# Performance work log

Measured on AMD Instinct MI355X. Metric: run time of the kernel, lower is better.

Reference implementation:

```python
import jax, jax.numpy as jnp
import numpy as np

B, S, D, H = 2, 2048, 1024, 16
HD = D // H  # head_dim = 64

def setup_inputs() -> dict:
    key = jax.random.key(0)
    ks = jax.random.split(key, 5)
    scale = 0.02
    return {
        "x":  jax.random.normal(ks[0], (B, S, D), dtype=jnp.float32),
        "Wq": jax.random.normal(ks[1], (D, D), dtype=jnp.float32) * scale,
        "Wk": jax.random.normal(ks[2], (D, D), dtype=jnp.float32) * scale,
        "Wv": jax.random.normal(ks[3], (D, D), dtype=jnp.float32) * scale,
        "Wo": jax.random.normal(ks[4], (D, D), dtype=jnp.float32) * scale,
    }

def reference(x, Wq, Wk, Wv, Wo):
    b, s, d = x.shape
    # projections (bias-free linear): [b,s,d] @ [d,d]
    q = (x @ Wq).reshape(b, s, H, HD).transpose(0, 2, 1, 3)  # [b,h,s,hd]
    k = (x @ Wk).reshape(b, s, H, HD).transpose(0, 2, 1, 3)
    v = (x @ Wv).reshape(b, s, H, HD).transpose(0, 2, 1, 3)
    scale = jnp.asarray(1.0 / np.sqrt(HD), dtype=x.dtype)
    scores = jnp.einsum('bhqd,bhkd->bhqk', q, k) * scale  # [b,h,s,s]
    causal = jnp.tril(jnp.ones((s, s), dtype=bool))
    scores = jnp.where(causal, scores, jnp.asarray(-jnp.inf, dtype=scores.dtype))
    attn = jax.nn.softmax(scores, axis=-1)
    out = jnp.einsum('bhqk,bhkd->bhqd', attn, v)  # [b,h,s,hd]
    out = out.transpose(0, 2, 1, 3).reshape(b, s, d)
    return out @ Wo
```

## Files before the change

kernel.cpp:

```cpp
#include <hip/hip_runtime.h>
#include <hip/hip_bf16.h>
#include <cstdint>

typedef __bf16 bf16;
typedef bf16 bf16x8 __attribute__((ext_vector_type(8)));
typedef bf16 bf16x4 __attribute__((ext_vector_type(4)));
typedef float f32x4 __attribute__((ext_vector_type(4)));

#define MFMA16(a, b, c) __builtin_amdgcn_mfma_f32_16x16x32_bf16(a, b, c, 0, 0, 0)

struct rawF { f32x4 a, b; };
__device__ inline rawF ldr(const float* p) {
  rawF r; r.a = *(const f32x4*)p; r.b = *(const f32x4*)(p + 4); return r;
}
__device__ inline bf16x8 ldr(const bf16* p) { return *(const bf16x8*)p; }
__device__ inline bf16x8 cv(const rawF& r) {
  bf16x8 o;
#pragma unroll
  for (int i = 0; i < 4; ++i) { o[i] = (bf16)r.a[i]; o[i + 4] = (bf16)r.b[i]; }
  return o;
}
__device__ inline bf16x8 cv(const bf16x8& r) { return r; }
__device__ inline void stC(bf16* C, size_t i, float v) { C[i] = (bf16)v; }
__device__ inline void stC(float* C, size_t i, float v) { C[i] = v; }

__device__ inline void gl16(const bf16* g, bf16* l) {
  __builtin_amdgcn_global_load_lds(
      (const __attribute__((address_space(1))) void*)g,
      (__attribute__((address_space(3))) void*)l, 16, 0, 0);
}

__device__ inline size_t tile_el(int rowg, int colg) {
  int kq = (colg >> 3) & 3;
  int s = (rowg & 15) ^ kq;
  return ((size_t)(rowg >> 7) * 32 + (colg >> 5)) * 4096 +
         (((rowg >> 6) & 1) << 11) + (((rowg >> 4) & 3) << 9) + (kq << 7) +
         (s << 3) + (colg & 7);
}

__global__ __launch_bounds__(256) void prep_wt(const float* __restrict__ W0,
                                               const float* __restrict__ W1,
                                               const float* __restrict__ W2,
                                               const float* __restrict__ W3,
                                               bf16* __restrict__ Wt, int n) {
  const float* Ws[4] = {W0, W1, W2, W3};
  const float* W = Ws[blockIdx.z];
  bf16* out = Wt + (size_t)blockIdx.z * n * n;
  __shared__ bf16 t[32][33];
  int bx = blockIdx.x * 32, by = blockIdx.y * 32;
  int tx = threadIdx.x & 31, ty = threadIdx.x >> 5;
#pragma unroll
  for (int i = 0; i < 32; i += 8)
    t[ty + i][tx] = (bf16)W[(size_t)(by + ty + i) * n + bx + tx];
  __syncthreads();
#pragma unroll
  for (int i = 0; i < 32; i += 8)
    out[(size_t)(bx + ty + i) * n + by + tx] = t[tx][ty + i];
}

__global__ __launch_bounds__(256) void prep_wt_t(const float* __restrict__ W0,
                                                 const float* __restrict__ W1,
                                                 const float* __restrict__ W2,
                                                 const float* __restrict__ W3,
                                                 bf16* __restrict__ Wt, int n) {
  const float* Ws[4] = {W0, W1, W2, W3};
  const float* W = Ws[blockIdx.z];
  bf16* out = Wt + (size_t)blockIdx.z * n * n;
  __shared__ bf16 t[32][33];
  int bx = blockIdx.x * 32, by = blockIdx.y * 32;
  int tx = threadIdx.x & 31, ty = threadIdx.x >> 5;
#pragma unroll
  for (int i = 0; i < 32; i += 8)
    t[ty + i][tx] = (bf16)W[(size_t)(by + ty + i) * n + bx + tx];
  __syncthreads();
#pragma unroll
  for (int i = 0; i < 32; i += 8) {
    int ng = bx + ty + i, kg = by + tx;
    out[tile_el(ng, kg)] = t[tx][ty + i];
  }
}

__global__ __launch_bounds__(256) void xcvt(const float* __restrict__ x, bf16* __restrict__ Xt) {
  int rbk = blockIdx.x, ks = blockIdx.y, t = threadIdx.x;
  int row = t >> 1, half = t & 1;
  const float* src = x + (size_t)(rbk * 128 + row) * 1024 + ks * 32 + half * 16;
  f32x4 v0 = *(const f32x4*)src;
  f32x4 v1 = *(const f32x4*)(src + 4);
  f32x4 v2 = *(const f32x4*)(src + 8);
  f32x4 v3 = *(const f32x4*)(src + 12);
  bf16* tile = Xt + ((size_t)rbk * 32 + ks) * 4096;
  int rb = (row >> 6) & 1, ii = (row >> 4) & 3;
#pragma unroll
  for (int u = 0; u < 2; ++u) {
    int kq = half * 2 + u;
    int s = (row & 15) ^ kq;
    const f32x4& a = u ? v2 : v0;
    const f32x4& b = u ? v3 : v1;
    bf16x8 o;
#pragma unroll
    for (int j = 0; j < 4; ++j) { o[j] = (bf16)a[j]; o[4 + j] = (bf16)b[j]; }
    *(bf16x8*)&tile[(rb << 11) | (ii << 9) | (kq << 7) | (s << 3)] = o;
  }
}

__global__ __launch_bounds__(256) void vtrans(const bf16* __restrict__ V, bf16* __restrict__ Vt) {
  constexpr int Sn = 2048, Dn = 1024;
  __shared__ bf16 L[64 * 66];
  int s0 = blockIdx.x * 64, bh = blockIdx.y;
  int b = bh >> 4, h = bh & 15;
  int t = threadIdx.x;
  int r = t >> 3, c8 = (t & 7) * 8;
#pragma unroll
  for (int half = 0; half < 2; ++half) {
    int rr = r + half * 32;
    bf16x8 v = *(const bf16x8*)&V[(size_t)(b * Sn + s0 + rr) * Dn + h * 64 + c8];
#pragma unroll
    for (int j = 0; j < 8; ++j) L[(c8 + j) * 66 + rr] = v[j];
  }
  __syncthreads();
  int hd = t >> 3;
#pragma unroll
  for (int half = 0; half < 2; ++half) {
    int hh = hd + half * 32;
    bf16x8 o;
#pragma unroll
    for (int j = 0; j < 8; ++j) o[j] = L[hh * 66 + c8 + j];
    *(bf16x8*)&Vt[(size_t)bh * 64 * Sn + (size_t)hh * Sn + s0 + c8] = o;
  }
}

template <typename TC>
__global__ __launch_bounds__(256) void gemmT(const bf16* __restrict__ At,
                                             const bf16* __restrict__ B0,
                                             const bf16* __restrict__ B1,
                                             const bf16* __restrict__ B2,
                                             TC* __restrict__ C0, TC* __restrict__ C1,
                                             TC* __restrict__ C2, int nsteps, int nblk) {
  __shared__ bf16 As[2][4096];
  __shared__ bf16 Bs[2][4096];
  int tid = threadIdx.x, wave = tid >> 6, lane = tid & 63;
  int la = lane & 15, quad = lane >> 4;
  int by = blockIdx.y, sel = by / nblk, nb = by - sel * nblk;
  const bf16* Bt = sel == 0 ? B0 : (sel == 1 ? B1 : B2);
  TC* C = sel == 0 ? C0 : (sel == 1 ? C1 : C2);
  const bf16* Atb = At + (size_t)blockIdx.x * nsteps * 4096;
  const bf16* Btb = Bt + (size_t)nb * nsteps * 4096;
  int so = wave * 512 + lane * 8;
  int rdA = (wave >> 1) * 2048 + quad * 128 + ((la ^ quad) * 8);
  int rdB = (wave & 1) * 2048 + quad * 128 + ((la ^ quad) * 8);

  f32x4 zero = {0.f, 0.f, 0.f, 0.f};
  f32x4 acc[4][4];
#pragma unroll
  for (int i = 0; i < 4; ++i)
#pragma unroll
    for (int j = 0; j < 4; ++j) acc[i][j] = zero;

  {
    const bf16* ga = Atb;
    const bf16* gb = Btb;
    gl16(ga + so, &As[0][so]);
    gl16(ga + so + 2048, &As[0][so + 2048]);
    gl16(gb + so, &Bs[0][so]);
    gl16(gb + so + 2048, &Bs[0][so + 2048]);
  }
  int cur = 0;
  for (int ks = 0; ks < nsteps; ++ks) {
    __syncthreads();
    if (ks + 1 < nsteps) {
      const bf16* ga = Atb + (size_t)(ks + 1) * 4096;
      const bf16* gb = Btb + (size_t)(ks + 1) * 4096;
      gl16(ga + so, &As[cur ^ 1][so]);
      gl16(ga + so + 2048, &As[cur ^ 1][so + 2048]);
      gl16(gb + so, &Bs[cur ^ 1][so]);
      gl16(gb + so + 2048, &Bs[cur ^ 1][so + 2048]);
    }
    bf16x8 af[4], bfr[4];
#pragma unroll
    for (int i = 0; i < 4; ++i) af[i] = *(const bf16x8*)&As[cur][rdA + i * 512];
#pragma unroll
    for (int j = 0; j < 4; ++j) bfr[j] = *(const bf16x8*)&Bs[cur][rdB + j * 512];
#pragma unroll
    for (int i = 0; i < 4; ++i)
#pragma unroll
      for (int j = 0; j < 4; ++j) acc[i][j] = MFMA16(af[i], bfr[j], acc[i][j]);
    cur ^= 1;
  }
#pragma unroll
  for (int i = 0; i < 4; ++i) {
#pragma unroll
    for (int j = 0; j < 4; ++j) {
      int col = nb * 128 + (wave & 1) * 64 + j * 16 + la;
#pragma unroll
      for (int r = 0; r < 4; ++r) {
        int row = blockIdx.x * 128 + (wave >> 1) * 64 + i * 16 + quad * 4 + r;
        stC(C, (size_t)row * 1024 + col, acc[i][j][r]);
      }
    }
  }
}

template <typename TA, typename TC, bool BT>
__global__ __launch_bounds__(256) void gemm3(const TA* __restrict__ A,
                                             const void* __restrict__ B0p,
                                             const void* __restrict__ B1p,
                                             const void* __restrict__ B2p,
                                             TC* __restrict__ C0, TC* __restrict__ C1,
                                             TC* __restrict__ C2, int M, int N, int K, int nblk) {
  constexpr int LDA = 40;
  __shared__ bf16 As[BT ? 4096 : 5120];
  __shared__ bf16 Bs[4096];
  int tid = threadIdx.x, wave = tid >> 6, lane = tid & 63;
  int la = lane & 15, quad = lane >> 4;
  int wr = (wave >> 1) * 64, wc = (wave & 1) * 64;
  int by = blockIdx.y;
  int sel = by / nblk;
  int n0 = (by - sel * nblk) * 128;
  const void* Bp = sel == 0 ? B0p : (sel == 1 ? B1p : B2p);
  TC* C = sel == 0 ? C0 : (sel == 1 ? C1 : C2);
  const TA* Ab = A + (size_t)blockIdx.x * 128 * K;
  using TB = typename std::conditional<BT, bf16, float>::type;
  const TB* Bm = (const TB*)Bp;

  int ar[2], ac[2], br[2], bc[2], swz[2];
  int sq = tid & 3;
#pragma unroll
  for (int p = 0; p < 2; ++p) {
    int li = (tid + p * 256) * 8;
    ar[p] = li >> 5; ac[p] = li & 31;
    if (BT) { br[p] = li >> 5; bc[p] = li & 31; }
    else    { br[p] = li >> 7; bc[p] = li & 127; }
    int row = ar[p];
    swz[p] = ((row >> 6) << 12) | (((row >> 4) & 3) << 10) | (sq << 8) |
             ((((row & 15) ^ sq)) << 4);
  }
  int rdA = (wave >> 1) * 4096 + quad * 256 + ((la ^ quad) << 4);
  int rdB = (wave & 1) * 4096 + quad * 256 + ((la ^ quad) << 4);

  f32x4 zero = {0.f, 0.f, 0.f, 0.f};
  f32x4 acc[4][4];
#pragma unroll
  for (int i = 0; i < 4; ++i)
#pragma unroll
    for (int j = 0; j < 4; ++j) acc[i][j] = zero;

  decltype(ldr((const TA*)nullptr)) pa[2];
  decltype(ldr((const TB*)nullptr)) pb[2];
#pragma unroll
  for (int p = 0; p < 2; ++p) {
    pa[p] = ldr(&Ab[(size_t)ar[p] * K + ac[p]]);
    if (BT) pb[p] = ldr(&Bm[(size_t)(n0 + br[p]) * K + bc[p]]);
    else    pb[p] = ldr(&Bm[(size_t)br[p] * N + n0 + bc[p]]);
  }

  for (int k0 = 0; k0 < K; k0 += 32) {
#pragma unroll
    for (int p = 0; p < 2; ++p) {
      if constexpr (BT) {
        *(bf16x8*)((char*)As + swz[p]) = cv(pa[p]);
        *(bf16x8*)((char*)Bs + swz[p]) = cv(pb[p]);
      } else {
        *(bf16x8*)&As[ar[p] * LDA + ac[p]] = cv(pa[p]);
        bf16x8 v = cv(pb[p]);
        int kx = br[p] ^ (((bc[p] >> 3) & 3) << 3);
#pragma unroll
        for (int j = 0; j < 8; ++j) Bs[(bc[p] + j) * 32 + kx] = v[j];
      }
    }
    __syncthreads();
    int k1 = k0 + 32;
    if (k1 < K) {
#pragma unroll
      for (int p = 0; p < 2; ++p) {
        pa[p] = ldr(&Ab[(size_t)ar[p] * K + k1 + ac[p]]);
        if (BT) pb[p] = ldr(&Bm[(size_t)(n0 + br[p]) * K + k1 + bc[p]]);
        else    pb[p] = ldr(&Bm[(size_t)(k1 + br[p]) * N + n0 + bc[p]]);
      }
    }
    bf16x8 af[4], bfr[4];
#pragma unroll
    for (int i = 0; i < 4; ++i) {
      if constexpr (BT)
        af[i] = *(const bf16x8*)((const char*)As + rdA + i * 1024);
      else
        af[i] = *(const bf16x8*)&As[(wr + i * 16 + la) * LDA + quad * 8];
    }
#pragma unroll
    for (int j = 0; j < 4; ++j) {
      if constexpr (BT) {
        bfr[j] = *(const bf16x8*)((const char*)Bs + rdB + j * 1024);
      } else {
        int nr = wc + j * 16 + la;
        bfr[j] = *(const bf16x8*)&Bs[nr * 32 + ((quad * 8) ^ (((nr >> 3) & 3) << 3))];
      }
    }
#pragma unroll
    for (int i = 0; i < 4; ++i)
#pragma unroll
      for (int j = 0; j < 4; ++j) acc[i][j] = MFMA16(af[i], bfr[j], acc[i][j]);
    __syncthreads();
  }
#pragma unroll
  for (int i = 0; i < 4; ++i) {
#pragma unroll
    for (int j = 0; j < 4; ++j) {
      int col = n0 + wc + j * 16 + la;
#pragma unroll
      for (int r = 0; r < 4; ++r) {
        int row = blockIdx.x * 128 + wr + i * 16 + quad * 4 + r;
        stC(C, (size_t)row * N + col, acc[i][j][r]);
      }
    }
  }
}

template <bool OT>
__global__ __launch_bounds__(256) void flash_attn(const bf16* __restrict__ Q,
                                                  const bf16* __restrict__ Kg,
                                                  const bf16* __restrict__ Vtg,
                                                  bf16* __restrict__ O,
                                                  bf16* __restrict__ Ot) {
  constexpr int D = 1024, S = 2048;
  const float MASK = -3.0e4f;
  const float SCL2 = 0.18033688011112042f;
  __shared__ bf16 Ks[4096];
  __shared__ bf16 Vs[4096];
  __shared__ bf16 Ps[4096];

  int n = blockIdx.x;
  int bh = n & 31;
  int j5 = n >> 5;
  int j = j5 & 15;
  int qt = (j5 & 16) ? j : 31 - j;
  int b = bh >> 4, h = bh & 15;
  int tid = threadIdx.x, wave = tid >> 6, lane = tid & 63;
  int la = lane & 15, quad = lane >> 4;
  const size_t base = (size_t)b * S * D + (size_t)h * 64;
  const bf16* Qg = Q + base;
  const bf16* Kb = Kg + base;
  const bf16* Vb = Vtg + (size_t)bh * 64 * S;
  int r0 = tid >> 3, c0 = (tid & 7) * 8;

  int quads = (tid & 7) & 3, kcs = (tid & 7) >> 2;
  int st0 = (r0 >> 4) * 1024 + kcs * 512 + quads * 128 +
            (((r0 & 15) ^ quads ^ (kcs << 2)) * 8);
  int kvrd0 = quad * 128 + ((la ^ quad) * 8);
  int kvrd1 = 512 + quad * 128 + ((la ^ quad ^ 4) * 8);
  int prd0 = wave * 1024 + quad * 128 + ((la ^ ((quad & 1) << 2)) * 8);
  int prd1 = prd0 + 512;
  int pwb = wave * 1024 + (quad >> 1) * 128 +
            ((la ^ ((quad >> 1) << 2)) * 8) + (quad & 1) * 4;

  f32x4 zero = {0.f, 0.f, 0.f, 0.f};
  int q0 = qt * 64;
  int ntiles = qt + 1;

  bf16x8 aq[2];
  {
    int qrow = q0 + wave * 16 + la;
#pragma unroll
    for (int kc = 0; kc < 2; ++kc) {
      bf16x8 t = *(const bf16x8*)&Qg[(size_t)qrow * D + kc * 32 + quad * 8];
#pragma unroll
      for (int i = 0; i < 8; ++i) t[i] = (bf16)((float)t[i] * SCL2);
      aq[kc] = t;
    }
  }

  f32x4 o[4];
#pragma unroll
  for (int nt = 0; nt < 4; ++nt) o[nt] = zero;
  float m_l = MASK, l_l = 0.f;

  bf16x8 kr0 = *(const bf16x8*)&Kb[(size_t)r0 * D + c0];
  bf16x8 kr1 = *(const bf16x8*)&Kb[(size_t)(r0 + 32) * D + c0];
  bf16x8 vr0 = *(const bf16x8*)&Vb[(size_t)r0 * S + c0];
  bf16x8 vr1 = *(const bf16x8*)&Vb[(size_t)(r0 + 32) * S + c0];

  for (int t = 0; t < ntiles; ++t) {
    *(bf16x8*)&Ks[st0] = kr0;
    *(bf16x8*)&Ks[st0 + 2048] = kr1;
    *(bf16x8*)&Vs[st0] = vr0;
    *(bf16x8*)&Vs[st0 + 2048] = vr1;
    __syncthreads();
    if (t + 1 < ntiles) {
      int kb2 = (t + 1) * 64;
      kr0 = *(const bf16x8*)&Kb[(size_t)(kb2 + r0) * D + c0];
      kr1 = *(const bf16x8*)&Kb[(size_t)(kb2 + r0 + 32) * D + c0];
      vr0 = *(const bf16x8*)&Vb[(size_t)r0 * S + kb2 + c0];
      vr1 = *(const bf16x8*)&Vb[(size_t)(r0 + 32) * S + kb2 + c0];
    }

    f32x4 s[4];
    __builtin_amdgcn_s_setprio(1);
#pragma unroll
    for (int nt = 0; nt < 4; ++nt) {
      bf16x8 k0f = *(const bf16x8*)&Ks[nt * 1024 + kvrd0];
      bf16x8 k1f = *(const bf16x8*)&Ks[nt * 1024 + kvrd1];
      f32x4 z = zero;
      z = MFMA16(k0f, aq[0], z);
      z = MFMA16(k1f, aq[1], z);
      s[nt] = z;
    }
    __builtin_amdgcn_s_setprio(0);

    if (t == qt) {
      int qa = q0 + wave * 16 + la;
      int kb = t * 64;
#pragma unroll
      for (int nt = 0; nt < 4; ++nt)
#pragma unroll
        for (int r = 0; r < 4; ++r) {
          int ka = kb + nt * 16 + quad * 4 + r;
          s[nt][r] = (ka > qa) ? MASK : s[nt][r];
        }
    }

    float mx;
    {
      float u0 = fmaxf(fmaxf(s[0][0], s[0][1]), fmaxf(s[0][2], s[0][3]));
      float u1 = fmaxf(fmaxf(s[1][0], s[1][1]), fmaxf(s[1][2], s[1][3]));
      float u2 = fmaxf(fmaxf(s[2][0], s[2][1]), fmaxf(s[2][2], s[2][3]));
      float u3 = fmaxf(fmaxf(s[3][0], s[3][1]), fmaxf(s[3][2], s[3][3]));
      mx = fmaxf(fmaxf(u0, u1), fmaxf(u2, u3));
    }
    mx = fmaxf(mx, m_l);
    mx = fmaxf(mx, __shfl_xor(mx, 16, 64));
    mx = fmaxf(mx, __shfl_xor(mx, 32, 64));

    if (!__all(mx - m_l <= 8.0f)) {
      float alpha = __builtin_amdgcn_exp2f(m_l - mx);
      m_l = mx;
      l_l *= alpha;
      float ab[4];
#pragma unroll
      for (int r = 0; r < 4; ++r) ab[r] = __shfl(alpha, quad * 4 + r, 64);
#pragma unroll
      for (int nt = 0; nt < 4; ++nt)
#pragma unroll
        for (int r = 0; r < 4; ++r) o[nt][r] *= ab[r];
    }

    float rs = 0.f;
#pragma unroll
    for (int nt = 0; nt < 4; ++nt) {
      float p0 = __builtin_amdgcn_exp2f(s[nt][0] - m_l);
      float p1 = __builtin_amdgcn_exp2f(s[nt][1] - m_l);
      float p2 = __builtin_amdgcn_exp2f(s[nt][2] - m_l);
      float p3 = __builtin_amdgcn_exp2f(s[nt][3] - m_l);
      s[nt][0] = p0; s[nt][1] = p1; s[nt][2] = p2; s[nt][3] = p3;
      rs += (p0 + p1) + (p2 + p3);
    }
    rs += __shfl_xor(rs, 16, 64);
    rs += __shfl_xor(rs, 32, 64);
    l_l += rs;

#pragma unroll
    for (int nt = 0; nt < 4; ++nt) {
      bf16x4 pk;
#pragma unroll
      for (int r = 0; r < 4; ++r) pk[r] = (bf16)s[nt][r];
      *(bf16x4*)&Ps[pwb + nt * 256] = pk;
    }

    __builtin_amdgcn_s_setprio(1);
    {
      bf16x8 ap0 = *(const bf16x8*)&Ps[prd0];
#pragma unroll
      for (int nt = 0; nt < 4; ++nt) {
        bf16x8 bv = *(const bf16x8*)&Vs[nt * 1024 + kvrd0];
        o[nt] = MFMA16(ap0, bv, o[nt]);
      }
      bf16x8 ap1 = *(const bf16x8*)&Ps[prd1];
#pragma unroll
      for (int nt = 0; nt < 4; ++nt) {
        bf16x8 bv = *(const bf16x8*)&Vs[nt * 1024 + kvrd1];
        o[nt] = MFMA16(ap1, bv, o[nt]);
      }
    }
    __builtin_amdgcn_s_setprio(0);
    __syncthreads();
  }

  float inv[4];
#pragma unroll
  for (int r = 0; r < 4; ++r) {
    float lv = __shfl(l_l, quad * 4 + r, 64);
    inv[r] = (lv > 1e-30f) ? 1.0f / lv : 0.0f;
  }
#pragma unroll
  for (int nt = 0; nt < 4; ++nt) {
    int hd = nt * 16 + la;
#pragma unroll
    for (int r = 0; r < 4; ++r) {
      int row = q0 + wave * 16 + quad * 4 + r;
      float v = o[nt][r] * inv[r];
      if (OT) {
        int rowg = b * S + row, colg = h * 64 + hd;
        Ot[tile_el(rowg, colg)] = (bf16)v;
      } else {
        O[base + (size_t)row * D + hd] = (bf16)v;
      }
    }
  }
}

extern "C" void kernel_launch(void* const* d_in, const int* in_sizes, int n_in,
                              void* d_out, int out_size, void* d_ws, size_t ws_size,
                              hipStream_t stream) {
  constexpr int B = 2, S = 2048, D = 1024;
  constexpr int M = B * S;
  constexpr size_t WN = (size_t)D * D;
  constexpr size_t XN = (size_t)M * D;

  const float* x = (const float*)d_in[0];
  const float* Wq = (const float*)d_in[1];
  const float* Wk = (const float*)d_in[2];
  const float* Wv = (const float*)d_in[3];
  const float* Wo = (const float*)d_in[4];
  float* out = (float*)d_out;

  if (ws_size < 2 * XN * sizeof(bf16)) return;
  bf16* Qb = (bf16*)d_ws;
  bf16* Vtg = Qb + XN;
  bf16* Wt = Vtg + XN;
  bf16* Xt = Wt + 4 * WN;
  bf16* Kb = (bf16*)d_out;
  bf16* Vb = Kb + XN;
  bool use_bt = ws_size >= (2 * XN + 4 * WN) * sizeof(bf16);
  bool big_ws = ws_size >= (3 * XN + 4 * WN) * sizeof(bf16);

  if (big_ws) {
    prep_wt_t<<<dim3(32, 32, 4), 256, 0, stream>>>(Wq, Wk, Wv, Wo, Wt, D);
    xcvt<<<dim3(32, 32), 256, 0, stream>>>(x, Xt);
    gemmT<bf16><<<dim3(M / 128, 24), 256, 0, stream>>>(Xt, Wt, Wt + WN, Wt + 2 * WN,
                                                       Qb, Kb, Vb, 32, 8);
    vtrans<<<dim3(S / 64, 32), 256, 0, stream>>>(Vb, Vtg);
    flash_attn<true><<<dim3(1024), 256, 0, stream>>>(Qb, Kb, Vtg, nullptr, Xt);
    gemmT<float><<<dim3(M / 128, 8), 256, 0, stream>>>(Xt, Wt + 3 * WN, Wt + 3 * WN,
                                                       Wt + 3 * WN, out, out, out, 32, 8);
    return;
  }

  dim3 gq(M / 128, 24), gf(M / 128, 8);
  if (use_bt) {
    prep_wt<<<dim3(32, 32, 4), 256, 0, stream>>>(Wq, Wk, Wv, Wo, Wt, D);
    gemm3<float, bf16, true><<<gq, 256, 0, stream>>>(x, Wt, Wt + WN, Wt + 2 * WN,
                                                     Qb, Kb, Vb, M, D, D, 8);
  } else {
    gemm3<float, bf16, false><<<gq, 256, 0, stream>>>(x, Wq, Wk, Wv, Qb, Kb, Vb, M, D, D, 8);
  }
  vtrans<<<dim3(S / 64, 32), 256, 0, stream>>>(Vb, Vtg);
  flash_attn<false><<<dim3(1024), 256, 0, stream>>>(Qb, Kb, Vtg, Qb, nullptr);
  if (use_bt) {
    gemm3<bf16, float, true><<<gf, 256, 0, stream>>>(Qb, Wt + 3 * WN, Wt + 3 * WN, Wt + 3 * WN,
                                                     out, out, out, M, D, D, 8);
  } else {
    gemm3<bf16, float, false><<<gf, 256, 0, stream>>>(Qb, Wo, Wo, Wo, out, out, out, M, D, D, 8);
  }
}
```

Baseline: 176.7 us.

## Fuse x fp32-to-bf16 conversion into QKV GEMM and double-buffer attention K/V

Removes the separate xcvt kernel: a new gemmTh GEMM loads fp32 x directly from global memory, converts it to bf16 in registers and writes it to swizzled LDS. The weight-transpose kernel now writes 16-byte vector stores instead of scalar ones. Flash attention double-buffers its K/V LDS tiles so the trailing barrier per tile can be dropped, and the softmax rescale and output normalization are vectorized. The fused GEMM reads fp32 x 24 times across the N-blocks instead of bf16 tiles once, which costs extra bandwidth and register pressure.

```diff
diff --git a/kernel.cpp b/kernel.cpp
--- a/kernel.cpp
+++ b/kernel.cpp
@@ -73,33 +73,13 @@
   for (int i = 0; i < 32; i += 8)
     t[ty + i][tx] = (bf16)W[(size_t)(by + ty + i) * n + bx + tx];
   __syncthreads();
-#pragma unroll
-  for (int i = 0; i < 32; i += 8) {
-    int ng = bx + ty + i, kg = by + tx;
-    out[tile_el(ng, kg)] = t[tx][ty + i];
-  }
-}
-
-__global__ __launch_bounds__(256) void xcvt(const float* __restrict__ x, bf16* __restrict__ Xt) {
-  int rbk = blockIdx.x, ks = blockIdx.y, t = threadIdx.x;
-  int row = t >> 1, half = t & 1;
-  const float* src = x + (size_t)(rbk * 128 + row) * 1024 + ks * 32 + half * 16;
-  f32x4 v0 = *(const f32x4*)src;
-  f32x4 v1 = *(const f32x4*)(src + 4);
-  f32x4 v2 = *(const f32x4*)(src + 8);
-  f32x4 v3 = *(const f32x4*)(src + 12);
-  bf16* tile = Xt + ((size_t)rbk * 32 + ks) * 4096;
-  int rb = (row >> 6) & 1, ii = (row >> 4) & 3;
-#pragma unroll
-  for (int u = 0; u < 2; ++u) {
-    int kq = half * 2 + u;
-    int s = (row & 15) ^ kq;
-    const f32x4& a = u ? v2 : v0;
-    const f32x4& b = u ? v3 : v1;
+  int tid = threadIdx.x;
+  if (tid < 128) {
+    int ngl = tid >> 2, kc0 = (tid & 3) * 8;
     bf16x8 o;
 #pragma unroll
-    for (int j = 0; j < 4; ++j) { o[j] = (bf16)a[j]; o[4 + j] = (bf16)b[j]; }
-    *(bf16x8*)&tile[(rb << 11) | (ii << 9) | (kq << 7) | (s << 3)] = o;
+    for (int j = 0; j < 8; ++j) o[j] = t[kc0 + j][ngl];
+    *(bf16x8*)&out[tile_el(bx + ngl, by + kc0)] = o;
   }
 }
 
@@ -126,6 +106,86 @@
 #pragma unroll
     for (int j = 0; j < 8; ++j) o[j] = L[hh * 66 + c8 + j];
     *(bf16x8*)&Vt[(size_t)bh * 64 * Sn + (size_t)hh * Sn + s0 + c8] = o;
+  }
+}
+
+template <typename TC>
+__global__ __launch_bounds__(256) void gemmTh(const float* __restrict__ A,
+                                              const bf16* __restrict__ B0,
+                                              const bf16* __restrict__ B1,
+                                              const bf16* __restrict__ B2,
+                                              TC* __restrict__ C0, TC* __restrict__ C1,
+                                              TC* __restrict__ C2, int nsteps, int nblk) {
+  __shared__ bf16 As[2][4096];
+  __shared__ bf16 Bs[2][4096];
+  int tid = threadIdx.x, wave = tid >> 6, lane = tid & 63;
+  int la = lane & 15, quad = lane >> 4;
+  int by = blockIdx.y, sel = by / nblk, nb = by - sel * nblk;
+  const bf16* Bt = sel == 0 ? B0 : (sel == 1 ? B1 : B2);
+  TC* C = sel == 0 ? C0 : (sel == 1 ? C1 : C2);
+  const float* Ab = A + (size_t)blockIdx.x * 128 * 1024;
+  const bf16* Btb = Bt + (size_t)nb * nsteps * 4096;
+  int so = wave * 512 + lane * 8;
+
+  int ar[2], ac[2], swz[2];
+  int sq = tid & 3;
+#pragma unroll
+  for (int p = 0; p < 2; ++p) {
+    int li = (tid + p * 256) * 8;
+    ar[p] = li >> 5; ac[p] = li & 31;
+    swz[p] = ((ar[p] >> 6) << 12) | (((ar[p] >> 4) & 3) << 10) | (sq << 8) |
+             (((ar[p] & 15) ^ sq) << 4);
+  }
+  int rdA = (wave >> 1) * 2048 + quad * 128 + ((la ^ quad) * 8);
+  int rdB = (wave & 1) * 2048 + quad * 128 + ((la ^ quad) * 8);
+
+  f32x4 zero = {0.f, 0.f, 0.f, 0.f};
+  f32x4 acc[4][4];
+#pragma unroll
+  for (int i = 0; i < 4; ++i)
+#pragma unroll
+    for (int j = 0; j < 4; ++j) acc[i][j] = zero;
+
+  rawF pa[2];
+#pragma unroll
+  for (int p = 0; p < 2; ++p) pa[p] = ldr(&Ab[(size_t)ar[p] * 1024 + ac[p]]);
+  gl16(Btb + so, &Bs[0][so]);
+  gl16(Btb + so + 2048, &Bs[0][so + 2048]);
+
+  for (int ks = 0; ks < nsteps; ++ks) {
+    int cur = ks & 1;
+    *(bf16x8*)((char*)&As[cur][0] + swz[0]) = cv(pa[0]);
+    *(bf16x8*)((char*)&As[cur][0] + swz[1]) = cv(pa[1]);
+    __syncthreads();
+    if (ks + 1 < nsteps) {
+      int kc = (ks + 1) * 32;
+#pragma unroll
+      for (int p = 0; p < 2; ++p) pa[p] = ldr(&Ab[(size_t)ar[p] * 1024 + kc + ac[p]]);
+      const bf16* gb = Btb + (size_t)(ks + 1) * 4096;
+      gl16(gb + so, &Bs[cur ^ 1][so]);
+      gl16(gb + so + 2048, &Bs[cur ^ 1][so + 2048]);
+    }
+    bf16x8 af[4], bfr[4];
+#pragma unroll
+    for (int i = 0; i < 4; ++i) af[i] = *(const bf16x8*)&As[cur][rdA + i * 512];
+#pragma unroll
+    for (int j = 0; j < 4; ++j) bfr[j] = *(const bf16x8*)&Bs[cur][rdB + j * 512];
+#pragma unroll
+    for (int i = 0; i < 4; ++i)
+#pragma unroll
+      for (int j = 0; j < 4; ++j) acc[i][j] = MFMA16(af[i], bfr[j], acc[i][j]);
+  }
+#pragma unroll
+  for (int i = 0; i < 4; ++i) {
+#pragma unroll
+    for (int j = 0; j < 4; ++j) {
+      int col = nb * 128 + (wave & 1) * 64 + j * 16 + la;
+#pragma unroll
+      for (int r = 0; r < 4; ++r) {
+        int row = blockIdx.x * 128 + (wave >> 1) * 64 + i * 16 + quad * 4 + r;
+        stC(C, (size_t)row * 1024 + col, acc[i][j][r]);
+      }
+    }
   }
 }
 
@@ -156,14 +216,11 @@
 #pragma unroll
     for (int j = 0; j < 4; ++j) acc[i][j] = zero;
 
-  {
-    const bf16* ga = Atb;
-    const bf16* gb = Btb;
-    gl16(ga + so, &As[0][so]);
-    gl16(ga + so + 2048, &As[0][so + 2048]);
-    gl16(gb + so, &Bs[0][so]);
-    gl16(gb + so + 2048, &Bs[0][so + 2048]);
-  }
+  gl16(Atb + so, &As[0][so]);
+  gl16(Atb + so + 2048, &As[0][so + 2048]);
+  gl16(Btb + so, &Bs[0][so]);
+  gl16(Btb + so + 2048, &Bs[0][so + 2048]);
+
   int cur = 0;
   for (int ks = 0; ks < nsteps; ++ks) {
     __syncthreads();
@@ -323,8 +380,8 @@
   constexpr int D = 1024, S = 2048;
   const float MASK = -3.0e4f;
   const float SCL2 = 0.18033688011112042f;
-  __shared__ bf16 Ks[4096];
-  __shared__ bf16 Vs[4096];
+  __shared__ bf16 Ks[2][4096];
+  __shared__ bf16 Vs[2][4096];
   __shared__ bf16 Ps[4096];
 
   int n = blockIdx.x;
@@ -378,10 +435,11 @@
   bf16x8 vr1 = *(const bf16x8*)&Vb[(size_t)(r0 + 32) * S + c0];
 
   for (int t = 0; t < ntiles; ++t) {
-    *(bf16x8*)&Ks[st0] = kr0;
-    *(bf16x8*)&Ks[st0 + 2048] = kr1;
-    *(bf16x8*)&Vs[st0] = vr0;
-    *(bf16x8*)&Vs[st0 + 2048] = vr1;
+    int cur = t & 1;
+    *(bf16x8*)&Ks[cur][st0] = kr0;
+    *(bf16x8*)&Ks[cur][st0 + 2048] = kr1;
+    *(bf16x8*)&Vs[cur][st0] = vr0;
+    *(bf16x8*)&Vs[cur][st0 + 2048] = vr1;
     __syncthreads();
     if (t + 1 < ntiles) {
       int kb2 = (t + 1) * 64;
@@ -395,8 +453,8 @@
     __builtin_amdgcn_s_setprio(1);
 #pragma unroll
     for (int nt = 0; nt < 4; ++nt) {
-      bf16x8 k0f = *(const bf16x8*)&Ks[nt * 1024 + kvrd0];
-      bf16x8 k1f = *(const bf16x8*)&Ks[nt * 1024 + kvrd1];
+      bf16x8 k0f = *(const bf16x8*)&Ks[cur][nt * 1024 + kvrd0];
+      bf16x8 k1f = *(const bf16x8*)&Ks[cur][nt * 1024 + kvrd1];
       f32x4 z = zero;
       z = MFMA16(k0f, aq[0], z);
       z = MFMA16(k1f, aq[1], z);
@@ -432,22 +490,22 @@
       float alpha = __builtin_amdgcn_exp2f(m_l - mx);
       m_l = mx;
       l_l *= alpha;
-      float ab[4];
-#pragma unroll
-      for (int r = 0; r < 4; ++r) ab[r] = __shfl(alpha, quad * 4 + r, 64);
-#pragma unroll
-      for (int nt = 0; nt < 4; ++nt)
-#pragma unroll
-        for (int r = 0; r < 4; ++r) o[nt][r] *= ab[r];
-    }
-
+      f32x4 abv;
+#pragma unroll
+      for (int r = 0; r < 4; ++r) abv[r] = __shfl(alpha, quad * 4 + r, 64);
+#pragma unroll
+      for (int nt = 0; nt < 4; ++nt) o[nt] *= abv;
+    }
+
+    f32x4 mlv = {m_l, m_l, m_l, m_l};
     float rs = 0.f;
 #pragma unroll
     for (int nt = 0; nt < 4; ++nt) {
-      float p0 = __builtin_amdgcn_exp2f(s[nt][0] - m_l);
-      float p1 = __builtin_amdgcn_exp2f(s[nt][1] - m_l);
-      float p2 = __builtin_amdgcn_exp2f(s[nt][2] - m_l);
-      float p3 = __builtin_amdgcn_exp2f(s[nt][3] - m_l);
+      f32x4 d = s[nt] - mlv;
+      float p0 = __builtin_amdgcn_exp2f(d[0]);
+      float p1 = __builtin_amdgcn_exp2f(d[1]);
+      float p2 = __builtin_amdgcn_exp2f(d[2]);
+      float p3 = __builtin_amdgcn_exp2f(d[3]);
       s[nt][0] = p0; s[nt][1] = p1; s[nt][2] = p2; s[nt][3] = p3;
       rs += (p0 + p1) + (p2 + p3);
     }
@@ -468,38 +526,37 @@
       bf16x8 ap0 = *(const bf16x8*)&Ps[prd0];
 #pragma unroll
       for (int nt = 0; nt < 4; ++nt) {
-        bf16x8 bv = *(const bf16x8*)&Vs[nt * 1024 + kvrd0];
+        bf16x8 bv = *(const bf16x8*)&Vs[cur][nt * 1024 + kvrd0];
         o[nt] = MFMA16(ap0, bv, o[nt]);
       }
       bf16x8 ap1 = *(const bf16x8*)&Ps[prd1];
 #pragma unroll
       for (int nt = 0; nt < 4; ++nt) {
-        bf16x8 bv = *(const bf16x8*)&Vs[nt * 1024 + kvrd1];
+        bf16x8 bv = *(const bf16x8*)&Vs[cur][nt * 1024 + kvrd1];
         o[nt] = MFMA16(ap1, bv, o[nt]);
       }
     }
     __builtin_amdgcn_s_setprio(0);
-    __syncthreads();
-  }
-
-  float inv[4];
+  }
+
+  f32x4 invv;
 #pragma unroll
   for (int r = 0; r < 4; ++r) {
     float lv = __shfl(l_l, quad * 4 + r, 64);
-    inv[r] = (lv > 1e-30f) ? 1.0f / lv : 0.0f;
+    invv[r] = (lv > 1e-30f) ? 1.0f / lv : 0.0f;
   }
 #pragma unroll
   for (int nt = 0; nt < 4; ++nt) {
+    o[nt] *= invv;
     int hd = nt * 16 + la;
 #pragma unroll
     for (int r = 0; r < 4; ++r) {
       int row = q0 + wave * 16 + quad * 4 + r;
-      float v = o[nt][r] * inv[r];
       if (OT) {
         int rowg = b * S + row, colg = h * 64 + hd;
-        Ot[tile_el(rowg, colg)] = (bf16)v;
+        Ot[tile_el(rowg, colg)] = (bf16)o[nt][r];
       } else {
-        O[base + (size_t)row * D + hd] = (bf16)v;
+        O[base + (size_t)row * D + hd] = (bf16)o[nt][r];
       }
     }
   }
@@ -524,7 +581,7 @@
   bf16* Qb = (bf16*)d_ws;
   bf16* Vtg = Qb + XN;
   bf16* Wt = Vtg + XN;
-  bf16* Xt = Wt + 4 * WN;
+  bf16* Ot = Wt + 4 * WN;
   bf16* Kb = (bf16*)d_out;
   bf16* Vb = Kb + XN;
   bool use_bt = ws_size >= (2 * XN + 4 * WN) * sizeof(bf16);
@@ -532,12 +589,11 @@
 
   if (big_ws) {
     prep_wt_t<<<dim3(32, 32, 4), 256, 0, stream>>>(Wq, Wk, Wv, Wo, Wt, D);
-    xcvt<<<dim3(32, 32), 256, 0, stream>>>(x, Xt);
-    gemmT<bf16><<<dim3(M / 128, 24), 256, 0, stream>>>(Xt, Wt, Wt + WN, Wt + 2 * WN,
-                                                       Qb, Kb, Vb, 32, 8);
+    gemmTh<bf16><<<dim3(M / 128, 24), 256, 0, stream>>>(x, Wt, Wt + WN, Wt + 2 * WN,
+                                                        Qb, Kb, Vb, 32, 8);
     vtrans<<<dim3(S / 64, 32), 256, 0, stream>>>(Vb, Vtg);
-    flash_attn<true><<<dim3(1024), 256, 0, stream>>>(Qb, Kb, Vtg, nullptr, Xt);
-    gemmT<float><<<dim3(M / 128, 8), 256, 0, stream>>>(Xt, Wt + 3 * WN, Wt + 3 * WN,
+    flash_attn<true><<<dim3(1024), 256, 0, stream>>>(Qb, Kb, Vtg, nullptr, Ot);
+    gemmT<float><<<dim3(M / 128, 8), 256, 0, stream>>>(Ot, Wt + 3 * WN, Wt + 3 * WN,
                                                        Wt + 3 * WN, out, out, out, 32, 8);
     return;
   }
```

Result: slower. 187.0 us (+5.8%).
